# Performance work log

Hardware: AMD Instinct MI355X
Metric: run time of the kernel (lower is better)

## Reference

```python
import jax, jax.numpy as jnp
import numpy as np

NUM_CLASSES = 20
MEM_SIZE = 512      # memory_bank_size
MAX_VIEWS = 512
TEMP = 0.1
MOMENTUM = 0.999
IGNORE_IDX = 255
AUX_IDX = 254
EPS = 1e-12


def _nearest_resize(gt, Ho, Wo):
    # torch F.interpolate(mode='nearest'): src = floor(dst * in/out)
    B, Hi, Wi = gt.shape
    ri = (jnp.arange(Ho) * Hi) // Ho
    ci = (jnp.arange(Wo) * Wi) // Wo
    return gt[:, ri][:, :, ci]


def _norm_flat(p):
    # L2-normalize over channels, then [B, C, H, W] -> [B, H*W, C]
    p = p / jnp.maximum(jnp.linalg.norm(p, axis=1, keepdims=True), EPS)
    B, C = p.shape[0], p.shape[1]
    return p.reshape(B, C, -1).transpose(0, 2, 1)


def setup_inputs() -> dict:
    key = jax.random.key(0)
    k1, k2, k3, k4, k5 = jax.random.split(key, 5)
    B, D, H, W = 4, 256, 128, 128
    Hg, Wg = 512, 512
    return {
        'main_proj': jax.random.normal(k1, (B, D, H, W), dtype=jnp.float32),
        'main_gt': jax.random.randint(k2, (B, Hg, Wg), 0, NUM_CLASSES).astype(jnp.int64),
        'aux_proj': jax.random.normal(k3, (B, D, H, W), dtype=jnp.float32),
        'aux_gt': jax.random.randint(k4, (B, Hg, Wg), 0, NUM_CLASSES).astype(jnp.int64),
        'memory_bank': jax.random.normal(k5, (NUM_CLASSES, MEM_SIZE, D), dtype=jnp.float32),
    }


def reference(main_proj, main_gt, aux_proj, aux_gt, memory_bank):
    C, M, D = memory_bank.shape
    B, _, H, W = main_proj.shape
    mg = _nearest_resize(main_gt, H, W)
    ag = _nearest_resize(aux_gt, aux_proj.shape[2], aux_proj.shape[3])

    embd = jnp.concatenate([_norm_flat(main_proj), _norm_flat(aux_proj)], axis=1)
    embd = embd.reshape(-1, D)                       # [N, D]
    label = jnp.concatenate([mg.reshape(B, -1), ag.reshape(B, -1)], axis=1).reshape(-1)

    valid = label != IGNORE_IDX
    label = jnp.where(label == AUX_IDX, C - 1, label)

    # per-class gather: stable argsort puts class-c pixels first (deterministic
    # stand-in for torch.randperm selection)
    masks = (label[None, :] == jnp.arange(C)[:, None]) & valid[None, :]   # [C, N]
    counts = masks.sum(axis=1)                                           # [C]
    order = jnp.argsort(~masks, axis=1, stable=True)[:, :M]              # [C, M]
    sel = embd[order]                                                    # [C, M, D]
    sel_valid = jnp.arange(M)[None, :] < counts[:, None]                 # [C, M]

    # momentum scatter-update to memory bank (no grad through features)
    upd = MOMENTUM * memory_bank + (1.0 - MOMENTUM) * jax.lax.stop_gradient(sel)
    upd = upd / jnp.maximum(jnp.linalg.norm(upd, axis=2, keepdims=True), EPS)
    bank = jnp.where(sel_valid[..., None], upd, memory_bank)             # [C, M, D]

    # anchors from current batch (with grad)
    V = min(MAX_VIEWS, M)
    anchors = sel[:, :V].reshape(C * V, D)
    a_valid = sel_valid[:, :V].reshape(-1)
    a_lbl = jnp.repeat(jnp.arange(C), V)

    # contrastive samples from updated bank (constant w.r.t. grad)
    contras = bank.reshape(C * M, D)
    c_valid = jnp.linalg.norm(bank, axis=2).reshape(-1) > 0
    c_lbl = jnp.repeat(jnp.arange(C), M)

    # InfoNCE with masked softmax over valid contrastive columns
    scores = (anchors @ contras.T) / TEMP                                # [A, K]
    scores = jnp.where(c_valid[None, :], scores, -1e9)
    logp = jax.nn.log_softmax(scores, axis=1)
    pos = ((a_lbl[:, None] == c_lbl[None, :]) & c_valid[None, :]).astype(scores.dtype)
    pos_sum = (pos * logp).sum(axis=1)
    pos_cnt = pos.sum(axis=1)
    va = (pos_cnt > 0) & a_valid
    mlpp = jnp.where(va, pos_sum / jnp.maximum(pos_cnt, 1.0), 0.0)
    loss = -mlpp.sum() / jnp.maximum(va.sum(), 1).astype(scores.dtype)
    return loss
```

## Files before the change

kernel.cpp:

```cpp
#include <hip/hip_runtime.h>
#include <cstdint>
#include <math.h>

#define NCLS  20
#define MSZ   512
#define DIM   256
#define HW    16384
#define NPIX  131072
#define AROWS 10240
#define TEMP_INV 10.0f
#define EXP2K 14.4269504088896f

typedef __attribute__((ext_vector_type(8))) short bf16x8;
typedef __attribute__((ext_vector_type(4))) float f32x4;

__device__ __forceinline__ short f2bf(float f) {
    unsigned u = __float_as_uint(f);
    unsigned r = (u + 0x7FFFu + ((u >> 16) & 1u)) >> 16;
    return (short)r;
}
__device__ __forceinline__ float bf2f(short s) {
    return __uint_as_float(((unsigned)(unsigned short)s) << 16);
}
__device__ __forceinline__ float fexp2(float x) {
    float r;
    asm volatile("v_exp_f32 %0, %1" : "=v"(r) : "v"(x));
    return r;
}
__device__ __forceinline__ void gld16(const void* g, void* l) {
    __builtin_amdgcn_global_load_lds(
        (const __attribute__((address_space(1))) unsigned int*)(uintptr_t)g,
        (__attribute__((address_space(3))) unsigned int*)(unsigned int)(uintptr_t)l,
        16, 0, 0);
}

#define ZREG_FLOATS 15488

__global__ __launch_bounds__(256) void k_hist(const int* __restrict__ mg,
                                              const int* __restrict__ ag,
                                              int* __restrict__ labels,
                                              int* __restrict__ hist,
                                              int* __restrict__ pix2row,
                                              float* __restrict__ zreg) {
    int chunk = blockIdx.x, t = threadIdx.x;
    int lane = t & 63;
    int gi = chunk * 256 + t;
    if (gi < ZREG_FLOATS) zreg[gi] = 0.0f;

    int n = gi;
    int b = n >> 15, r = n & 32767;
    const int* g = (r < HW) ? mg : ag;
    int p = (r < HW) ? r : (r - HW);
    int h = p >> 7, w = p & 127;
    int lab = g[(((size_t)b * 512) + (size_t)(h << 2)) * 512 + (size_t)(w << 2)];
    if (lab == 255) lab = -1;
    else if (lab == 254) lab = NCLS - 1;
    labels[n] = lab;
    pix2row[n] = -1;

    __shared__ int cnt20[NCLS];
    if (t < NCLS) cnt20[t] = 0;
    __syncthreads();
#pragma unroll
    for (int c = 0; c < NCLS; ++c) {
        unsigned long long m = __ballot(lab == c);
        if (lane == 0 && m) atomicAdd(&cnt20[c], __popcll(m));
    }
    __syncthreads();
    if (t < NCLS) hist[t * 512 + chunk] = cnt20[t];
}

__global__ __launch_bounds__(256) void k_write(const int* __restrict__ labels,
                                               const int* __restrict__ hist,
                                               int* __restrict__ pix2row,
                                               int* __restrict__ counts) {
    int chunk = blockIdx.x, t = threadIdx.x;
    int lane = t & 63, wv = t >> 6;
    __shared__ int cbase[NCLS];
    __shared__ int wcnt2[4][NCLS];

#pragma unroll
    for (int cc = 0; cc < 5; ++cc) {
        int c = wv * 5 + cc;
        int s = 0;
        for (int j = lane; j < chunk; j += 64) s += hist[c * 512 + j];
#pragma unroll
        for (int o = 32; o > 0; o >>= 1) s += __shfl_down(s, o, 64);
        if (lane == 0) cbase[c] = s;
    }

    int n = chunk * 256 + t;
    int lab = labels[n];
    int myrank = 0;
#pragma unroll
    for (int c = 0; c < NCLS; ++c) {
        unsigned long long m = __ballot(lab == c);
        if (lane == 0) wcnt2[wv][c] = __popcll(m);
        if (lab == c) myrank = __popcll(m & ((1ull << lane) - 1ull));
    }
    __syncthreads();
    if (lab >= 0) {
        int base = cbase[lab] + myrank;
        for (int w = 0; w < wv; ++w) base += wcnt2[w][lab];
        if (base < MSZ) pix2row[n] = lab * MSZ + base;
    }
    if (chunk == 511 && t < NCLS)
        counts[t] = cbase[t] + wcnt2[0][t] + wcnt2[1][t] + wcnt2[2][t] + wcnt2[3][t];
}

__global__ __launch_bounds__(256) void k_scatter(const float* __restrict__ mainp,
                                                 const float* __restrict__ auxp,
                                                 const int* __restrict__ pix2row,
                                                 float* __restrict__ xF) {
    int idx = blockIdx.x * 256 + threadIdx.x;
    int p4 = idx & 4095;
    int ch = (idx >> 12) & 255;
    int bs = idx >> 20;
    int b = bs >> 1, src = bs & 1;
    const float* base = (src ? auxp : mainp) + (size_t)b * DIM * HW + (size_t)ch * HW;
    float4 v = *(const float4*)(base + p4 * 4);
    int4 pr = *(const int4*)(pix2row + bs * HW + p4 * 4);
    if (pr.x >= 0) xF[(size_t)pr.x * DIM + ch] = v.x;
    if (pr.y >= 0) xF[(size_t)pr.y * DIM + ch] = v.y;
    if (pr.z >= 0) xF[(size_t)pr.z * DIM + ch] = v.z;
    if (pr.w >= 0) xF[(size_t)pr.w * DIM + ch] = v.w;
}

__global__ __launch_bounds__(256) void k_nbc(const float* __restrict__ xF,
                                             const float* __restrict__ bank,
                                             const int* __restrict__ counts,
                                             short* __restrict__ anchorsB,
                                             short* __restrict__ contrasB,
                                             int* __restrict__ c_valid,
                                             float* __restrict__ S,
                                             int* __restrict__ pcnt) {
    int blk = blockIdx.x;
    int c = blk >> 3;
    int t = threadIdx.x, lane = t & 63, wv = t >> 6;
    int cc = counts[c];
    int base = blk * 64;
    float sacc[4] = {0.f, 0.f, 0.f, 0.f};
    int vcnt = 0;

    for (int it = 0; it < 16; ++it) {
        int a = base + it * 4 + wv;
        int m = a & 511;
        float4 xv = *(const float4*)&xF[(size_t)a * DIM + lane * 4];
        float x[4] = {xv.x, xv.y, xv.z, xv.w};
        float ss = x[0]*x[0] + x[1]*x[1] + x[2]*x[2] + x[3]*x[3];
#pragma unroll
        for (int o = 1; o < 64; o <<= 1) ss += __shfl_xor(ss, o, 64);
        float scale = 1.0f / fmaxf(sqrtf(ss), 1e-12f);
        float ax[4];
#pragma unroll
        for (int q = 0; q < 4; ++q) ax[q] = x[q] * scale;
        short4 oa;
        oa.x = f2bf(ax[0]); oa.y = f2bf(ax[1]); oa.z = f2bf(ax[2]); oa.w = f2bf(ax[3]);
        *(short4*)&anchorsB[(size_t)a * DIM + lane * 4] = oa;

        bool upd = m < cc;
        float4 bv = *(const float4*)&bank[(size_t)a * DIM + lane * 4];
        float u[4];
        u[0] = upd ? 0.999f * bv.x + 0.001f * ax[0] : bv.x;
        u[1] = upd ? 0.999f * bv.y + 0.001f * ax[1] : bv.y;
        u[2] = upd ? 0.999f * bv.z + 0.001f * ax[2] : bv.z;
        u[3] = upd ? 0.999f * bv.w + 0.001f * ax[3] : bv.w;
        float ss2 = u[0]*u[0] + u[1]*u[1] + u[2]*u[2] + u[3]*u[3];
#pragma unroll
        for (int o = 1; o < 64; o <<= 1) ss2 += __shfl_xor(ss2, o, 64);
        float nrm = sqrtf(ss2);
        float inv = 1.0f / fmaxf(nrm, 1e-12f);
        short oc[4];
        oc[0] = f2bf(upd ? u[0] * inv : bv.x);
        oc[1] = f2bf(upd ? u[1] * inv : bv.y);
        oc[2] = f2bf(upd ? u[2] * inv : bv.z);
        oc[3] = f2bf(upd ? u[3] * inv : bv.w);
        *(short4*)&contrasB[(size_t)a * DIM + lane * 4] = *(short4*)oc;
        bool valid = nrm > 0.0f;
        if (lane == 0) {
            c_valid[a] = valid ? 1 : 0;
            vcnt += valid ? 1 : 0;
        }
        if (valid) {
#pragma unroll
            for (int q = 0; q < 4; ++q) sacc[q] += bf2f(oc[q]);
        }
    }

    __shared__ float s4[4][DIM];
    __shared__ int pv[4];
#pragma unroll
    for (int q = 0; q < 4; ++q) s4[wv][lane * 4 + q] = sacc[q];
    if (lane == 0) pv[wv] = vcnt;
    __syncthreads();
    float s = s4[0][t] + s4[1][t] + s4[2][t] + s4[3][t];
    atomicAdd(&S[c * DIM + t], s);
    if (t == 0) atomicAdd(&pcnt[c], pv[0] + pv[1] + pv[2] + pv[3]);
}

__global__ __launch_bounds__(512, 2) void k_score(const short* __restrict__ A,
                                                  const short* __restrict__ Bc,
                                                  const int* __restrict__ c_valid,
                                                  float* __restrict__ row_sumexp) {
    __shared__ short lds[2][2][256 * 64];
    const int t = threadIdx.x;
    const int lane = t & 63, wv = t >> 6;
    const int wr = wv & 1, wc = wv >> 1;
    const int qr = lane >> 4, qc = lane & 15;
    const int s7 = qc & 7;
    const int row0 = blockIdx.x * 256, col0 = blockIdx.y * 256;

    const int rl = t >> 3;
    const int sdat = (t & 7) ^ (rl & 7);
    const short* Ag = A  + (size_t)row0 * DIM;
    const short* Bg = Bc + (size_t)col0 * DIM;

    const int sl0 = ((0 + qr) ^ s7) * 8;
    const int sl1 = ((4 + qr) ^ s7) * 8;

    f32x4 acc[2][2][4][2] = {};
    bf16x8 A0[4][2], A1[4][2], Bf[2][2];

    auto stage = [&](int buf, int kt) {
#pragma unroll
        for (int q = 0; q < 4; ++q)
            gld16(Ag + (size_t)(q * 64 + rl) * DIM + kt * 64 + sdat * 8,
                  &lds[buf][0][(q * 64 + wv * 8) * 64]);
#pragma unroll
        for (int q = 0; q < 4; ++q)
            gld16(Bg + (size_t)(q * 64 + rl) * DIM + kt * 64 + sdat * 8,
                  &lds[buf][1][(q * 64 + wv * 8) * 64]);
    };
    auto readA = [&](bf16x8 (&Af)[4][2], const short* base, int rh) {
#pragma unroll
        for (int rt = 0; rt < 4; ++rt) {
            const int rb = (wr * 128 + rh * 64 + rt * 16 + qc) * 64;
            Af[rt][0] = *(const bf16x8*)&base[rb + sl0];
            Af[rt][1] = *(const bf16x8*)&base[rb + sl1];
        }
    };
    auto readB = [&](const short* base, int ch) {
#pragma unroll
        for (int ct = 0; ct < 2; ++ct) {
            const int rb = (wc * 64 + ch * 32 + ct * 16 + qc) * 64;
            Bf[ct][0] = *(const bf16x8*)&base[rb + sl0];
            Bf[ct][1] = *(const bf16x8*)&base[rb + sl1];
        }
    };

#define BARR asm volatile("s_barrier" ::: "memory")
#define DOMFMA(RH, CH, AF)                                                               \
    _Pragma("unroll")                                                                    \
    for (int rt = 0; rt < 4; ++rt) {                                                     \
        _Pragma("unroll")                                                                \
        for (int ct = 0; ct < 2; ++ct) {                                                 \
            acc[RH][CH][rt][ct] = __builtin_amdgcn_mfma_f32_16x16x32_bf16(               \
                AF[rt][0], Bf[ct][0], acc[RH][CH][rt][ct], 0, 0, 0);                     \
            acc[RH][CH][rt][ct] = __builtin_amdgcn_mfma_f32_16x16x32_bf16(               \
                AF[rt][1], Bf[ct][1], acc[RH][CH][rt][ct], 0, 0, 0);                     \
        }                                                                                \
    }

    stage(0, 0);
#pragma unroll
    for (int kt = 0; kt < 4; ++kt) {
        const int buf = kt & 1;
        asm volatile("s_waitcnt vmcnt(0)" ::: "memory");
        BARR;
        if (kt < 3) stage(buf ^ 1, kt + 1);
        const short* Ab = &lds[buf][0][0];
        const short* Bb = &lds[buf][1][0];
        readA(A0, Ab, 0); readB(Bb, 0);
        BARR; __builtin_amdgcn_s_setprio(1); DOMFMA(0, 0, A0); __builtin_amdgcn_s_setprio(0); BARR;
        readB(Bb, 1);
        BARR; __builtin_amdgcn_s_setprio(1); DOMFMA(0, 1, A0); __builtin_amdgcn_s_setprio(0); BARR;
        readA(A1, Ab, 1);
        BARR; __builtin_amdgcn_s_setprio(1); DOMFMA(1, 1, A1); __builtin_amdgcn_s_setprio(0); BARR;
        readB(Bb, 0);
        BARR; __builtin_amdgcn_s_setprio(1); DOMFMA(1, 0, A1); __builtin_amdgcn_s_setprio(0); BARR;
    }
#undef DOMFMA
#undef BARR

    float cm[2][2];
#pragma unroll
    for (int ch = 0; ch < 2; ++ch)
#pragma unroll
        for (int ct = 0; ct < 2; ++ct)
            cm[ch][ct] = c_valid[col0 + wc * 64 + ch * 32 + ct * 16 + qc] ? 1.0f : 0.0f;
#pragma unroll
    for (int rh = 0; rh < 2; ++rh)
#pragma unroll
        for (int rt = 0; rt < 4; ++rt)
#pragma unroll
            for (int r = 0; r < 4; ++r) {
                float e = cm[0][0] * fexp2(acc[rh][0][rt][0][r] * EXP2K)
                        + cm[0][1] * fexp2(acc[rh][0][rt][1][r] * EXP2K)
                        + cm[1][0] * fexp2(acc[rh][1][rt][0][r] * EXP2K)
                        + cm[1][1] * fexp2(acc[rh][1][rt][1][r] * EXP2K);
#pragma unroll
                for (int o = 1; o < 16; o <<= 1) e += __shfl_xor(e, o, 64);
                if (qc == 0)
                    atomicAdd(&row_sumexp[row0 + wr * 128 + rh * 64 + rt * 16 + qr * 4 + r], e);
            }
}

__global__ __launch_bounds__(256) void k_fin(const short* __restrict__ anchorsB,
                                             const float* __restrict__ S,
                                             const int* __restrict__ counts,
                                             const int* __restrict__ pcnt,
                                             const float* __restrict__ row_sumexp,
                                             float* __restrict__ facc,
                                             int* __restrict__ done_cnt,
                                             float* __restrict__ out) {
    int blk = blockIdx.x;
    int c = blk >> 3;
    int t = threadIdx.x, lane = t & 63, wv = t >> 6;
    int pc = pcnt[c], cc = counts[c];
    float lsum = 0.0f, vc = 0.0f;

    for (int it = 0; it < 16; ++it) {
        int a = blk * 64 + it * 4 + wv;
        short4 a4 = *(const short4*)&anchorsB[(size_t)a * DIM + lane * 4];
        float4 s4 = *(const float4*)&S[c * DIM + lane * 4];
        float dot = bf2f(a4.x) * s4.x + bf2f(a4.y) * s4.y
                  + bf2f(a4.z) * s4.z + bf2f(a4.w) * s4.w;
#pragma unroll
        for (int o = 1; o < 64; o <<= 1) dot += __shfl_xor(dot, o, 64);
        if (lane == 0 && (a & 511) < cc && pc > 0) {
            float lse = logf(row_sumexp[a]);
            lsum += (TEMP_INV * dot - (float)pc * lse) / (float)pc;
            vc += 1.0f;
        }
    }

    __shared__ float wls[4], wvc[4];
    if (lane == 0) { wls[wv] = lsum; wvc[wv] = vc; }
    __syncthreads();
    if (t == 0) {
        atomicAdd(&facc[0], wls[0] + wls[1] + wls[2] + wls[3]);
        atomicAdd(&facc[1], wvc[0] + wvc[1] + wvc[2] + wvc[3]);
        __threadfence();
        unsigned d = atomicAdd((unsigned*)done_cnt, 1u);
        if (d == 159u) {
            __threadfence();
            float L = atomicAdd(&facc[0], 0.0f);
            float V = atomicAdd(&facc[1], 0.0f);
            out[0] = -L / fmaxf(V, 1.0f);
        }
    }
}

extern "C" void kernel_launch(void* const* d_in, const int* in_sizes, int n_in,
                              void* d_out, int out_size, void* d_ws, size_t ws_size,
                              hipStream_t stream) {
    const float* main_proj = (const float*)d_in[0];
    const int*   main_gt   = (const int*)d_in[1];
    const float* aux_proj  = (const float*)d_in[2];
    const int*   aux_gt    = (const int*)d_in[3];
    const float* bank      = (const float*)d_in[4];
    float* out = (float*)d_out;

    char* ws = (char*)d_ws;
    int*   labels     = (int*)ws;
    int*   hist       = (int*)(ws + 524288);
    int*   pix2row    = (int*)(ws + 565248);
    int*   c_valid    = (int*)(ws + 1089536);
    float* zreg       = (float*)(ws + 1130496);
    float* row_sumexp = zreg;
    float* S          = zreg + 10240;
    int*   pcnt       = (int*)(zreg + 15360);
    float* facc       = zreg + 15380;
    int*   done_cnt   = (int*)(zreg + 15382);
    int*   counts     = (int*)(ws + 1192448);
    float* xF         = (float*)(ws + 1192704);
    short* anchorsB   = (short*)(ws + 11678464);
    short* contrasB   = (short*)(ws + 16921344);

    k_hist<<<512, 256, 0, stream>>>(main_gt, aux_gt, labels, hist, pix2row, zreg);
    k_write<<<512, 256, 0, stream>>>(labels, hist, pix2row, counts);
    k_scatter<<<32768, 256, 0, stream>>>(main_proj, aux_proj, pix2row, xF);
    k_nbc<<<AROWS / 64, 256, 0, stream>>>(xF, bank, counts, anchorsB, contrasB,
                                          c_valid, S, pcnt);
    dim3 grid(AROWS / 256, AROWS / 256);
    k_score<<<grid, 512, 0, stream>>>(anchorsB, contrasB, c_valid, row_sumexp);
    k_fin<<<AROWS / 64, 256, 0, stream>>>(anchorsB, S, counts, pcnt, row_sumexp,
                                          facc, done_cnt, out);
}
```

Measured before the change: 320.6 us.

## Unroll GEMM k-loop with deeper prefetch and partial vmcnt waits

Manually unrolls the four k-tiles of the bf16 MFMA score GEMM. The next tile's global-to-LDS load is now issued before the current tile's wait, so the wait uses vmcnt(8) instead of draining all loads, keeping one tile's loads in flight during compute. It also separates the two B-fragment register sets, alternates the phase order between even and odd tiles, and fences the MFMA blocks with sched_barrier. This aims to hide global load latency behind MFMA work, at the cost of more live registers and a fixed, hand-ordered schedule.

Result: no change. 322.2 us (+0.5%).

```diff
diff --git a/kernel.cpp b/kernel.cpp
--- a/kernel.cpp
+++ b/kernel.cpp
@@ -219,7 +219,7 @@
     const int sl1 = ((4 + qr) ^ s7) * 8;
 
     f32x4 acc[2][2][4][2] = {};
-    bf16x8 A0[4][2], A1[4][2], Bf[2][2];
+    bf16x8 A0f[4][2], A1f[4][2], B0f[2][2], B1f[2][2];
 
     auto stage = [&](int buf, int kt) {
 #pragma unroll
@@ -239,47 +239,68 @@
             Af[rt][1] = *(const bf16x8*)&base[rb + sl1];
         }
     };
-    auto readB = [&](const short* base, int ch) {
+    auto readB = [&](bf16x8 (&Bfx)[2][2], const short* base, int ch) {
 #pragma unroll
         for (int ct = 0; ct < 2; ++ct) {
             const int rb = (wc * 64 + ch * 32 + ct * 16 + qc) * 64;
-            Bf[ct][0] = *(const bf16x8*)&base[rb + sl0];
-            Bf[ct][1] = *(const bf16x8*)&base[rb + sl1];
+            Bfx[ct][0] = *(const bf16x8*)&base[rb + sl0];
+            Bfx[ct][1] = *(const bf16x8*)&base[rb + sl1];
         }
     };
 
-#define BARR asm volatile("s_barrier" ::: "memory")
-#define DOMFMA(RH, CH, AF)                                                               \
+    const short* Ab0 = &lds[0][0][0];
+    const short* Bb0 = &lds[0][1][0];
+    const short* Ab1 = &lds[1][0][0];
+    const short* Bb1 = &lds[1][1][0];
+
+#define BARR   asm volatile("s_barrier" ::: "memory")
+#define VMW(N) asm volatile("s_waitcnt vmcnt(" #N ")" ::: "memory")
+#define MFMA16(RH, CH, AF, BF)                                                           \
     _Pragma("unroll")                                                                    \
     for (int rt = 0; rt < 4; ++rt) {                                                     \
         _Pragma("unroll")                                                                \
         for (int ct = 0; ct < 2; ++ct) {                                                 \
             acc[RH][CH][rt][ct] = __builtin_amdgcn_mfma_f32_16x16x32_bf16(               \
-                AF[rt][0], Bf[ct][0], acc[RH][CH][rt][ct], 0, 0, 0);                     \
+                AF[rt][0], BF[ct][0], acc[RH][CH][rt][ct], 0, 0, 0);                     \
             acc[RH][CH][rt][ct] = __builtin_amdgcn_mfma_f32_16x16x32_bf16(               \
-                AF[rt][1], Bf[ct][1], acc[RH][CH][rt][ct], 0, 0, 0);                     \
+                AF[rt][1], BF[ct][1], acc[RH][CH][rt][ct], 0, 0, 0);                     \
         }                                                                                \
     }
+#define PH(RH, CH, AF, BF)                                                               \
+    BARR;                                                                                \
+    __builtin_amdgcn_s_setprio(1);                                                       \
+    __builtin_amdgcn_sched_barrier(0);                                                   \
+    MFMA16(RH, CH, AF, BF);                                                              \
+    __builtin_amdgcn_sched_barrier(0);                                                   \
+    __builtin_amdgcn_s_setprio(0);                                                       \
+    BARR;
+
+#define KT_EVEN(AB, BB)                                                                  \
+    readA(A0f, AB, 0); readB(B0f, BB, 0); PH(0, 0, A0f, B0f)                             \
+    readB(B1f, BB, 1);                    PH(0, 1, A0f, B1f)                             \
+    readA(A1f, AB, 1);                    PH(1, 1, A1f, B1f)                             \
+    readB(B0f, BB, 0);                    PH(1, 0, A1f, B0f)
+#define KT_ODD(AB, BB)                                                                   \
+    readA(A0f, AB, 0); readB(B1f, BB, 1); PH(0, 1, A0f, B1f)                             \
+    readB(B0f, BB, 0);                    PH(0, 0, A0f, B0f)                             \
+    readA(A1f, AB, 1);                    PH(1, 0, A1f, B0f)                             \
+    readB(B1f, BB, 1);                    PH(1, 1, A1f, B1f)
 
     stage(0, 0);
-#pragma unroll
-    for (int kt = 0; kt < 4; ++kt) {
-        const int buf = kt & 1;
-        asm volatile("s_waitcnt vmcnt(0)" ::: "memory");
-        BARR;
-        if (kt < 3) stage(buf ^ 1, kt + 1);
-        const short* Ab = &lds[buf][0][0];
-        const short* Bb = &lds[buf][1][0];
-        readA(A0, Ab, 0); readB(Bb, 0);
-        BARR; __builtin_amdgcn_s_setprio(1); DOMFMA(0, 0, A0); __builtin_amdgcn_s_setprio(0); BARR;
-        readB(Bb, 1);
-        BARR; __builtin_amdgcn_s_setprio(1); DOMFMA(0, 1, A0); __builtin_amdgcn_s_setprio(0); BARR;
-        readA(A1, Ab, 1);
-        BARR; __builtin_amdgcn_s_setprio(1); DOMFMA(1, 1, A1); __builtin_amdgcn_s_setprio(0); BARR;
-        readB(Bb, 0);
-        BARR; __builtin_amdgcn_s_setprio(1); DOMFMA(1, 0, A1); __builtin_amdgcn_s_setprio(0); BARR;
-    }
-#undef DOMFMA
+    stage(1, 1); VMW(8); BARR;
+    KT_EVEN(Ab0, Bb0)
+    stage(0, 2); VMW(8); BARR;
+    KT_ODD(Ab1, Bb1)
+    stage(1, 3); VMW(8); BARR;
+    KT_EVEN(Ab0, Bb0)
+    VMW(0); BARR;
+    KT_ODD(Ab1, Bb1)
+
+#undef KT_ODD
+#undef KT_EVEN
+#undef PH
+#undef MFMA16
+#undef VMW
 #undef BARR
 
     float cm[2][2];
```
